# Optimization experiments

Hardware: AMD Instinct MI355X
Metric: run time of the kernel (lower is better)

The kernel has to match this reference:

```python
import jax, jax.numpy as jnp
import numpy as np

B, T, I, H, O, P = 32, 8192, 16, 128, 3, 1024


def setup_inputs() -> dict:
    key = jax.random.key(0)
    ks = jax.random.split(key, 8)
    x = jax.random.normal(ks[0], (B, T, I), dtype=jnp.float32)
    # feature channel 2 holds the photo id (original code does x[:,:,2].long())
    ids = jax.random.randint(ks[1], (B, T), 0, P)
    x = x.at[:, :, 2].set(ids.astype(jnp.float32))
    s = 1.0 / np.sqrt(H).astype(np.float32)
    W_ih = jax.random.uniform(ks[2], (4 * H, I), minval=-s, maxval=s, dtype=jnp.float32)
    W_hh = jax.random.uniform(ks[3], (4 * H, H), minval=-s, maxval=s, dtype=jnp.float32)
    b_ih = jax.random.uniform(ks[4], (4 * H,), minval=-s, maxval=s, dtype=jnp.float32)
    b_hh = jax.random.uniform(ks[5], (4 * H,), minval=-s, maxval=s, dtype=jnp.float32)
    W_fc = jax.random.uniform(ks[6], (O, H), minval=-s, maxval=s, dtype=jnp.float32)
    b_fc = jax.random.uniform(ks[7], (O,), minval=-s, maxval=s, dtype=jnp.float32)
    return dict(x=x, W_ih=W_ih, W_hh=W_hh, b_ih=b_ih, b_hh=b_hh,
                W_fc=W_fc, b_fc=b_fc, num_photos=P)


def _lstm(x, W_ih, W_hh, b_ih, b_hh):
    # single-layer batch_first LSTM, PyTorch gate order (i, f, g, o), zero init state
    Bz = x.shape[0]
    Hh = W_hh.shape[1]
    # precompute input contribution for all timesteps: [B, T, 4H]
    xg = jnp.einsum('bti,gi->btg', x, W_ih) + b_ih + b_hh

    def step(carry, gx):
        h, c = carry
        g = gx + h @ W_hh.T
        i, f, gg, o = jnp.split(g, 4, axis=-1)
        i = jax.nn.sigmoid(i)
        f = jax.nn.sigmoid(f)
        gg = jnp.tanh(gg)
        o = jax.nn.sigmoid(o)
        c = f * c + i * gg
        h = o * jnp.tanh(c)
        return (h, c), h

    h0 = jnp.zeros((Bz, Hh), x.dtype)
    _, hs = jax.lax.scan(step, (h0, h0), jnp.swapaxes(xg, 0, 1))  # [T, B, H]
    return jnp.swapaxes(hs, 0, 1)  # [B, T, H]


def reference(x, W_ih, W_hh, b_ih, b_hh, W_fc, b_fc, num_photos):
    Bz, T, _ = x.shape
    h = _lstm(x, W_ih, W_hh, b_ih, b_hh)          # [B, T, H]
    out = h @ W_fc.T + b_fc                        # [B, T, 3]
    ids = x[:, :, 2].astype(jnp.int32)             # [B, T]
    valid = ids < num_photos
    safe = jnp.where(valid, ids, 0)
    # flatten (batch, photo_id) into a single segment id per element
    seg = (jnp.arange(Bz, dtype=jnp.int32)[:, None] * num_photos + safe).reshape(-1)
    w = valid.astype(out.dtype)
    sums = jax.ops.segment_sum((out * w[..., None]).reshape(-1, out.shape[-1]),
                               seg, num_segments=Bz * num_photos)
    sums = sums.reshape(Bz, num_photos, out.shape[-1])
    counts = jax.ops.segment_sum(w.reshape(-1), seg, num_segments=Bz * num_photos)
    counts = counts.reshape(Bz, num_photos, 1)
    counts = jnp.where(counts == 0, 1.0, counts)   # matches photo_counts[photo_counts==0]=1
    return sums / counts
```

## Files before the change

### kernel.cpp

```cpp
#include <hip/hip_runtime.h>

#define B_ 32
#define T_ 8192
#define I_ 16
#define H_ 128
#define P_ 1024
#define O_ 3

typedef _Float16 h2 __attribute__((ext_vector_type(2)));
typedef _Float16 h4 __attribute__((ext_vector_type(4)));
typedef _Float16 h8 __attribute__((ext_vector_type(8)));

#if __has_builtin(__builtin_amdgcn_fdot2)
#define FDOT2(a, b, c) __builtin_amdgcn_fdot2((a), (b), (c), false)
#else
__device__ __forceinline__ float fdot2_asm(h2 a, h2 b, float c) {
    asm("v_dot2_f32_f16 %0, %1, %2, %0" : "+v"(c) : "v"(a), "v"(b));
    return c;
}
#define FDOT2(a, b, c) fdot2_asm((a), (b), (c))
#endif

#define FORME(M, g) M(g,0,0) M(g,0,1) M(g,0,2) M(g,0,3) \
                    M(g,1,0) M(g,1,1) M(g,1,2) M(g,1,3) \
                    M(g,2,0) M(g,2,1) M(g,2,2) M(g,2,3) \
                    M(g,3,0) M(g,3,1) M(g,3,2) M(g,3,3)
#define FORALL(M) FORME(M,0) FORME(M,1) FORME(M,2) FORME(M,3)
#define FORG(M) M(0) M(1) M(2) M(3)

#define DPPF(v, ctrl) \
    __int_as_float(__builtin_amdgcn_mov_dpp(__float_as_int(v), (ctrl), 0xF, 0xF, true))
#define SWZF(v, imm) \
    __int_as_float(__builtin_amdgcn_ds_swizzle(__float_as_int(v), (imm)))

__device__ __forceinline__ float tanh_f(float x) {
    return 2.f / (1.f + __expf(-2.f * x)) - 1.f;
}
__device__ __forceinline__ h4 cvt4(float4 v) {
    return (h4){(_Float16)v.x, (_Float16)v.y, (_Float16)v.z, (_Float16)v.w};
}

__device__ __forceinline__ void lds_barrier() {
    asm volatile("s_waitcnt lgkmcnt(0)\n\ts_barrier" ::: "memory");
}

__global__ __launch_bounds__(512, 2) __attribute__((amdgpu_waves_per_eu(2, 2)))
void lstm_fused(
    const float* __restrict__ x,
    const float* __restrict__ W_ih,
    const float* __restrict__ W_hh,
    const float* __restrict__ b_ih,
    const float* __restrict__ b_hh,
    const float* __restrict__ W_fc,
    float* __restrict__ sums,
    float* __restrict__ counts)
{
    const int b   = blockIdx.x;
    const int tid = threadIdx.x;
    const int j   = tid >> 2;
    const int kc  = tid & 3;

    __shared__ __align__(16) _Float16 hh[2][H_];
    __shared__ __align__(16) _Float16 xt[2][16 * I_];
    __shared__ float sums_lds[P_ * O_];
    __shared__ float counts_lds[P_];

    const float* wr0 = W_hh + (0 * H_ + j) * H_;
    const float* wr1 = W_hh + (1 * H_ + j) * H_;
    const float* wr2 = W_hh + (2 * H_ + j) * H_;
    const float* wr3 = W_hh + (3 * H_ + j) * H_;
    #define WLOAD(g, m, e) h2 W##g##_##m##_##e = (h2){ \
        (_Float16)wr##g[kc * 8 + 32 * (m) + 2 * (e)], \
        (_Float16)wr##g[kc * 8 + 32 * (m) + 2 * (e) + 1]};
    FORALL(WLOAD)

    #define ULOAD(g) \
        h2 U##g##_0 = (h2){(_Float16)W_ih[((g) * H_ + j) * I_ + kc * 4 + 0], \
                           (_Float16)W_ih[((g) * H_ + j) * I_ + kc * 4 + 1]}; \
        h2 U##g##_1 = (h2){(_Float16)W_ih[((g) * H_ + j) * I_ + kc * 4 + 2], \
                           (_Float16)W_ih[((g) * H_ + j) * I_ + kc * 4 + 3]};
    FORG(ULOAD)

    const float bias = b_ih[kc * H_ + j] + b_hh[kc * H_ + j];
    const float wfc  = (kc < 3) ? W_fc[kc * H_ + j] : 0.f;

    for (int i = tid; i < P_ * O_; i += 512) sums_lds[i] = 0.f;
    for (int i = tid; i < P_;      i += 512) counts_lds[i] = 0.f;
    if (tid < H_) hh[0][tid] = (_Float16)0.f;

    const float* xb = x + (size_t)b * T_ * I_;
    float4 xr4 = make_float4(0.f, 0.f, 0.f, 0.f);
    if (tid < 64) {
        xr4 = ((const float4*)xb)[tid];
        *(h4*)&xt[0][tid * 4] = cvt4(xr4);
    }
    float c = 0.f;
    __syncthreads();

    #pragma unroll 1
    for (int t = 0; t < T_; ++t) {
        const int off = t & 15;
        const int btx = (t >> 4) & 1;
        const int bh  = t & 1;

        if (tid < 64) {
            if (off == 0 && t + 16 < T_)
                xr4 = ((const float4*)(xb + (t + 16) * I_))[tid];
            if (off == 8 && t + 8 < T_)
                *(h4*)&xt[btx ^ 1][tid * 4] = cvt4(xr4);
        }

        const h4 xv4 = *(const h4*)&xt[btx][off * I_ + kc * 4];
        const h2 xv0 = __builtin_shufflevector(xv4, xv4, 0, 1);
        const h2 xv1 = __builtin_shufflevector(xv4, xv4, 2, 3);
        const int id = (int)(float)xt[btx][off * I_ + 2];

        float acc0 = 0.f, acc1 = 0.f, acc2 = 0.f, acc3 = 0.f;
        #define HD(m) { \
            h8 hv = *(const h8*)&hh[bh][kc * 8 + 32 * (m)]; \
            h2 p0 = __builtin_shufflevector(hv, hv, 0, 1); \
            h2 p1 = __builtin_shufflevector(hv, hv, 2, 3); \
            h2 p2 = __builtin_shufflevector(hv, hv, 4, 5); \
            h2 p3 = __builtin_shufflevector(hv, hv, 6, 7); \
            acc0 = FDOT2(p0, W0_##m##_0, acc0); acc0 = FDOT2(p1, W0_##m##_1, acc0); \
            acc0 = FDOT2(p2, W0_##m##_2, acc0); acc0 = FDOT2(p3, W0_##m##_3, acc0); \
            acc1 = FDOT2(p0, W1_##m##_0, acc1); acc1 = FDOT2(p1, W1_##m##_1, acc1); \
            acc1 = FDOT2(p2, W1_##m##_2, acc1); acc1 = FDOT2(p3, W1_##m##_3, acc1); \
            acc2 = FDOT2(p0, W2_##m##_0, acc2); acc2 = FDOT2(p1, W2_##m##_1, acc2); \
            acc2 = FDOT2(p2, W2_##m##_2, acc2); acc2 = FDOT2(p3, W2_##m##_3, acc2); \
            acc3 = FDOT2(p0, W3_##m##_0, acc3); acc3 = FDOT2(p1, W3_##m##_1, acc3); \
            acc3 = FDOT2(p2, W3_##m##_2, acc3); acc3 = FDOT2(p3, W3_##m##_3, acc3); }
        HD(0) HD(1) HD(2) HD(3)
        acc0 = FDOT2(xv0, U0_0, acc0); acc0 = FDOT2(xv1, U0_1, acc0);
        acc1 = FDOT2(xv0, U1_0, acc1); acc1 = FDOT2(xv1, U1_1, acc1);
        acc2 = FDOT2(xv0, U2_0, acc2); acc2 = FDOT2(xv1, U2_1, acc2);
        acc3 = FDOT2(xv0, U3_0, acc3); acc3 = FDOT2(xv1, U3_1, acc3);

        float s_;
        s_ = DPPF(acc0, 0xB1); acc0 += s_;
        s_ = DPPF(acc1, 0xB1); acc1 += s_;
        s_ = DPPF(acc2, 0xB1); acc2 += s_;
        s_ = DPPF(acc3, 0xB1); acc3 += s_;
        s_ = DPPF(acc0, 0x4E); acc0 += s_;
        s_ = DPPF(acc1, 0x4E); acc1 += s_;
        s_ = DPPF(acc2, 0x4E); acc2 += s_;
        s_ = DPPF(acc3, 0x4E); acc3 += s_;

        float tg = (kc == 0) ? acc0 : (kc == 1) ? acc1 : (kc == 2) ? acc2 : acc3;
        tg += bias;
        const bool  isg = (kc == 2);
        const float arg = isg ? (tg + tg) : tg;
        const float sf  = 1.f / (1.f + __expf(-arg));
        const float act = isg ? (sf + sf - 1.f) : sf;

        const float gi = DPPF(act, 0x00);
        const float gf = DPPF(act, 0x55);
        const float gg = DPPF(act, 0xAA);
        const float go = DPPF(act, 0xFF);
        c = fmaf(gf, c, gi * gg);
        const float hnew = go * tanh_f(c);

        if (kc == 0) hh[bh ^ 1][j] = (_Float16)hnew;

        float p = hnew * wfc;
        p += SWZF(p, 0x101F);
        p += SWZF(p, 0x201F);
        p += SWZF(p, 0x401F);
        p += __shfl_xor(p, 32, 64);
        const bool idv = ((unsigned)id < P_);
        if (((tid & 63) < 3) && idv)
            atomicAdd(&sums_lds[id * O_ + (tid & 63)], p);
        if (tid == 0 && idv)
            atomicAdd(&counts_lds[id], 1.f);

        lds_barrier();
    }

    float* sums_g = sums + (size_t)b * P_ * O_;
    for (int i = tid; i < P_ * O_; i += 512) sums_g[i] = sums_lds[i];
    float* cnt_g = counts + (size_t)b * P_;
    for (int i = tid; i < P_; i += 512) cnt_g[i] = counts_lds[i];
}

__global__ void finalize_kernel(const float* __restrict__ sums,
                                const float* __restrict__ counts,
                                const float* __restrict__ b_fc,
                                float* __restrict__ out)
{
    const int idx = blockIdx.x * blockDim.x + threadIdx.x;
    if (idx >= B_ * P_ * O_) return;
    const int o  = idx % O_;
    const int bp = idx / O_;
    const float cnt = counts[bp];
    const float denom = (cnt > 0.f) ? cnt : 1.f;
    out[idx] = (sums[idx] + cnt * b_fc[o]) / denom;
}

extern "C" void kernel_launch(void* const* d_in, const int* in_sizes, int n_in,
                              void* d_out, int out_size, void* d_ws, size_t ws_size,
                              hipStream_t stream) {
    const float* x    = (const float*)d_in[0];
    const float* W_ih = (const float*)d_in[1];
    const float* W_hh = (const float*)d_in[2];
    const float* b_ih = (const float*)d_in[3];
    const float* b_hh = (const float*)d_in[4];
    const float* W_fc = (const float*)d_in[5];
    const float* b_fc = (const float*)d_in[6];

    float* out    = (float*)d_out;
    float* sums   = (float*)d_ws;
    float* counts = sums + (size_t)B_ * P_ * O_;

    lstm_fused<<<B_, 512, 0, stream>>>(x, W_ih, W_hh, b_ih, b_hh, W_fc, sums, counts);

    const int n = B_ * P_ * O_;
    finalize_kernel<<<(n + 255) / 256, 256, 0, stream>>>(sums, counts, b_fc, out);
}
```

Baseline: 6.357 ms.

## Process two batch sequences per block with interleaved LSTM recurrences

Each block now runs two independent batch sequences, launched on 16 blocks instead of 32. Both recurrences are interleaved in one step loop so their dot products and reductions can hide each other's latency, and both share one barrier per timestep. The photo counts move out of the recurrent loop into a separate small count kernel. The trade-off is half as many blocks and roughly double the work per step, which may lengthen each serial step.

```diff
diff --git a/kernel.cpp b/kernel.cpp
--- a/kernel.cpp
+++ b/kernel.cpp
@@ -6,6 +6,7 @@
 #define H_ 128
 #define P_ 1024
 #define O_ 3
+#define NB 16
 
 typedef _Float16 h2 __attribute__((ext_vector_type(2)));
 typedef _Float16 h4 __attribute__((ext_vector_type(4)));
@@ -30,6 +31,7 @@
 
 #define DPPF(v, ctrl) \
     __int_as_float(__builtin_amdgcn_mov_dpp(__float_as_int(v), (ctrl), 0xF, 0xF, true))
+#define DPPI(v, ctrl) __builtin_amdgcn_mov_dpp((v), (ctrl), 0xF, 0xF, true)
 #define SWZF(v, imm) \
     __int_as_float(__builtin_amdgcn_ds_swizzle(__float_as_int(v), (imm)))
 
@@ -44,7 +46,7 @@
     asm volatile("s_waitcnt lgkmcnt(0)\n\ts_barrier" ::: "memory");
 }
 
-__global__ __launch_bounds__(512, 2) __attribute__((amdgpu_waves_per_eu(2, 2)))
+__global__ __launch_bounds__(512, 2)
 void lstm_fused(
     const float* __restrict__ x,
     const float* __restrict__ W_ih,
@@ -52,18 +54,22 @@
     const float* __restrict__ b_ih,
     const float* __restrict__ b_hh,
     const float* __restrict__ W_fc,
-    float* __restrict__ sums,
-    float* __restrict__ counts)
+    float* __restrict__ sums)
 {
-    const int b   = blockIdx.x;
-    const int tid = threadIdx.x;
-    const int j   = tid >> 2;
-    const int kc  = tid & 3;
-
-    __shared__ __align__(16) _Float16 hh[2][H_];
-    __shared__ __align__(16) _Float16 xt[2][16 * I_];
-    __shared__ float sums_lds[P_ * O_];
-    __shared__ float counts_lds[P_];
+    const int blk  = blockIdx.x;
+    const int tid  = threadIdx.x;
+    const int lane = tid & 63;
+    const int j    = tid >> 2;
+    const int kc   = tid & 3;
+    const int bA   = blk;
+    const int bB   = blk + NB;
+
+    __shared__ __align__(16) _Float16 hhA[2][H_];
+    __shared__ __align__(16) _Float16 hhB[2][H_];
+    __shared__ __align__(16) _Float16 xtA[2][16 * I_];
+    __shared__ __align__(16) _Float16 xtB[2][16 * I_];
+    __shared__ float sumsA_lds[P_ * O_];
+    __shared__ float sumsB_lds[P_ * O_];
 
     const float* wr0 = W_hh + (0 * H_ + j) * H_;
     const float* wr1 = W_hh + (1 * H_ + j) * H_;
@@ -73,7 +79,6 @@
         (_Float16)wr##g[kc * 8 + 32 * (m) + 2 * (e)], \
         (_Float16)wr##g[kc * 8 + 32 * (m) + 2 * (e) + 1]};
     FORALL(WLOAD)
-
     #define ULOAD(g) \
         h2 U##g##_0 = (h2){(_Float16)W_ih[((g) * H_ + j) * I_ + kc * 4 + 0], \
                            (_Float16)W_ih[((g) * H_ + j) * I_ + kc * 4 + 1]}; \
@@ -84,17 +89,16 @@
     const float bias = b_ih[kc * H_ + j] + b_hh[kc * H_ + j];
     const float wfc  = (kc < 3) ? W_fc[kc * H_ + j] : 0.f;
 
-    for (int i = tid; i < P_ * O_; i += 512) sums_lds[i] = 0.f;
-    for (int i = tid; i < P_;      i += 512) counts_lds[i] = 0.f;
-    if (tid < H_) hh[0][tid] = (_Float16)0.f;
-
-    const float* xb = x + (size_t)b * T_ * I_;
+    for (int i = tid; i < P_ * O_; i += 512) { sumsA_lds[i] = 0.f; sumsB_lds[i] = 0.f; }
+    if (tid < H_) { hhA[0][tid] = (_Float16)0.f; hhB[0][tid] = (_Float16)0.f; }
+
+    const float* xbA = x + (size_t)bA * T_ * I_;
+    const float* xbB = x + (size_t)bB * T_ * I_;
     float4 xr4 = make_float4(0.f, 0.f, 0.f, 0.f);
-    if (tid < 64) {
-        xr4 = ((const float4*)xb)[tid];
-        *(h4*)&xt[0][tid * 4] = cvt4(xr4);
-    }
-    float c = 0.f;
+    const int wv = tid >> 6;
+    if (wv == 0) { xr4 = ((const float4*)xbA)[lane]; *(h4*)&xtA[0][lane * 4] = cvt4(xr4); }
+    if (wv == 1) { xr4 = ((const float4*)xbB)[lane]; *(h4*)&xtB[0][lane * 4] = cvt4(xr4); }
+    float cA = 0.f, cB = 0.f;
     __syncthreads();
 
     #pragma unroll 1
@@ -103,83 +107,129 @@
         const int btx = (t >> 4) & 1;
         const int bh  = t & 1;
 
-        if (tid < 64) {
-            if (off == 0 && t + 16 < T_)
-                xr4 = ((const float4*)(xb + (t + 16) * I_))[tid];
-            if (off == 8 && t + 8 < T_)
-                *(h4*)&xt[btx ^ 1][tid * 4] = cvt4(xr4);
+        if (wv == 0) {
+            if (off == 0 && t + 16 < T_) xr4 = ((const float4*)(xbA + (t + 16) * I_))[lane];
+            if (off == 8 && t + 8 < T_)  *(h4*)&xtA[btx ^ 1][lane * 4] = cvt4(xr4);
+        } else if (wv == 1) {
+            if (off == 0 && t + 16 < T_) xr4 = ((const float4*)(xbB + (t + 16) * I_))[lane];
+            if (off == 8 && t + 8 < T_)  *(h4*)&xtB[btx ^ 1][lane * 4] = cvt4(xr4);
         }
 
-        const h4 xv4 = *(const h4*)&xt[btx][off * I_ + kc * 4];
-        const h2 xv0 = __builtin_shufflevector(xv4, xv4, 0, 1);
-        const h2 xv1 = __builtin_shufflevector(xv4, xv4, 2, 3);
-        const int id = (int)(float)xt[btx][off * I_ + 2];
-
-        float acc0 = 0.f, acc1 = 0.f, acc2 = 0.f, acc3 = 0.f;
-        #define HD(m) { \
-            h8 hv = *(const h8*)&hh[bh][kc * 8 + 32 * (m)]; \
-            h2 p0 = __builtin_shufflevector(hv, hv, 0, 1); \
-            h2 p1 = __builtin_shufflevector(hv, hv, 2, 3); \
-            h2 p2 = __builtin_shufflevector(hv, hv, 4, 5); \
-            h2 p3 = __builtin_shufflevector(hv, hv, 6, 7); \
-            acc0 = FDOT2(p0, W0_##m##_0, acc0); acc0 = FDOT2(p1, W0_##m##_1, acc0); \
-            acc0 = FDOT2(p2, W0_##m##_2, acc0); acc0 = FDOT2(p3, W0_##m##_3, acc0); \
-            acc1 = FDOT2(p0, W1_##m##_0, acc1); acc1 = FDOT2(p1, W1_##m##_1, acc1); \
-            acc1 = FDOT2(p2, W1_##m##_2, acc1); acc1 = FDOT2(p3, W1_##m##_3, acc1); \
-            acc2 = FDOT2(p0, W2_##m##_0, acc2); acc2 = FDOT2(p1, W2_##m##_1, acc2); \
-            acc2 = FDOT2(p2, W2_##m##_2, acc2); acc2 = FDOT2(p3, W2_##m##_3, acc2); \
-            acc3 = FDOT2(p0, W3_##m##_0, acc3); acc3 = FDOT2(p1, W3_##m##_1, acc3); \
-            acc3 = FDOT2(p2, W3_##m##_2, acc3); acc3 = FDOT2(p3, W3_##m##_3, acc3); }
-        HD(0) HD(1) HD(2) HD(3)
-        acc0 = FDOT2(xv0, U0_0, acc0); acc0 = FDOT2(xv1, U0_1, acc0);
-        acc1 = FDOT2(xv0, U1_0, acc1); acc1 = FDOT2(xv1, U1_1, acc1);
-        acc2 = FDOT2(xv0, U2_0, acc2); acc2 = FDOT2(xv1, U2_1, acc2);
-        acc3 = FDOT2(xv0, U3_0, acc3); acc3 = FDOT2(xv1, U3_1, acc3);
+        const h4 xA4 = *(const h4*)&xtA[btx][off * I_ + kc * 4];
+        const h4 xB4 = *(const h4*)&xtB[btx][off * I_ + kc * 4];
+        const h2 xA0 = __builtin_shufflevector(xA4, xA4, 0, 1);
+        const h2 xA1 = __builtin_shufflevector(xA4, xA4, 2, 3);
+        const h2 xB0 = __builtin_shufflevector(xB4, xB4, 0, 1);
+        const h2 xB1 = __builtin_shufflevector(xB4, xB4, 2, 3);
+        int idA = (int)(float)xA4[2]; idA = DPPI(idA, 0x00);
+        int idB = (int)(float)xB4[2]; idB = DPPI(idB, 0x00);
+
+        float a0A = 0.f, a1A = 0.f, a2A = 0.f, a3A = 0.f;
+        float a0B = 0.f, a1B = 0.f, a2B = 0.f, a3B = 0.f;
+        #define HD2(m) { \
+            h8 hA = *(const h8*)&hhA[bh][kc * 8 + 32 * (m)]; \
+            h8 hB = *(const h8*)&hhB[bh][kc * 8 + 32 * (m)]; \
+            h2 pA0 = __builtin_shufflevector(hA, hA, 0, 1); \
+            h2 pA1 = __builtin_shufflevector(hA, hA, 2, 3); \
+            h2 pA2 = __builtin_shufflevector(hA, hA, 4, 5); \
+            h2 pA3 = __builtin_shufflevector(hA, hA, 6, 7); \
+            h2 pB0 = __builtin_shufflevector(hB, hB, 0, 1); \
+            h2 pB1 = __builtin_shufflevector(hB, hB, 2, 3); \
+            h2 pB2 = __builtin_shufflevector(hB, hB, 4, 5); \
+            h2 pB3 = __builtin_shufflevector(hB, hB, 6, 7); \
+            a0A = FDOT2(pA0, W0_##m##_0, a0A); a0A = FDOT2(pA1, W0_##m##_1, a0A); \
+            a0A = FDOT2(pA2, W0_##m##_2, a0A); a0A = FDOT2(pA3, W0_##m##_3, a0A); \
+            a1A = FDOT2(pA0, W1_##m##_0, a1A); a1A = FDOT2(pA1, W1_##m##_1, a1A); \
+            a1A = FDOT2(pA2, W1_##m##_2, a1A); a1A = FDOT2(pA3, W1_##m##_3, a1A); \
+            a2A = FDOT2(pA0, W2_##m##_0, a2A); a2A = FDOT2(pA1, W2_##m##_1, a2A); \
+            a2A = FDOT2(pA2, W2_##m##_2, a2A); a2A = FDOT2(pA3, W2_##m##_3, a2A); \
+            a3A = FDOT2(pA0, W3_##m##_0, a3A); a3A = FDOT2(pA1, W3_##m##_1, a3A); \
+            a3A = FDOT2(pA2, W3_##m##_2, a3A); a3A = FDOT2(pA3, W3_##m##_3, a3A); \
+            a0B = FDOT2(pB0, W0_##m##_0, a0B); a0B = FDOT2(pB1, W0_##m##_1, a0B); \
+            a0B = FDOT2(pB2, W0_##m##_2, a0B); a0B = FDOT2(pB3, W0_##m##_3, a0B); \
+            a1B = FDOT2(pB0, W1_##m##_0, a1B); a1B = FDOT2(pB1, W1_##m##_1, a1B); \
+            a1B = FDOT2(pB2, W1_##m##_2, a1B); a1B = FDOT2(pB3, W1_##m##_3, a1B); \
+            a2B = FDOT2(pB0, W2_##m##_0, a2B); a2B = FDOT2(pB1, W2_##m##_1, a2B); \
+            a2B = FDOT2(pB2, W2_##m##_2, a2B); a2B = FDOT2(pB3, W2_##m##_3, a2B); \
+            a3B = FDOT2(pB0, W3_##m##_0, a3B); a3B = FDOT2(pB1, W3_##m##_1, a3B); \
+            a3B = FDOT2(pB2, W3_##m##_2, a3B); a3B = FDOT2(pB3, W3_##m##_3, a3B); }
+        HD2(0) HD2(1) HD2(2) HD2(3)
+        a0A = FDOT2(xA0, U0_0, a0A); a0A = FDOT2(xA1, U0_1, a0A);
+        a1A = FDOT2(xA0, U1_0, a1A); a1A = FDOT2(xA1, U1_1, a1A);
+        a2A = FDOT2(xA0, U2_0, a2A); a2A = FDOT2(xA1, U2_1, a2A);
+        a3A = FDOT2(xA0, U3_0, a3A); a3A = FDOT2(xA1, U3_1, a3A);
+        a0B = FDOT2(xB0, U0_0, a0B); a0B = FDOT2(xB1, U0_1, a0B);
+        a1B = FDOT2(xB0, U1_0, a1B); a1B = FDOT2(xB1, U1_1, a1B);
+        a2B = FDOT2(xB0, U2_0, a2B); a2B = FDOT2(xB1, U2_1, a2B);
+        a3B = FDOT2(xB0, U3_0, a3B); a3B = FDOT2(xB1, U3_1, a3B);
 
         float s_;
-        s_ = DPPF(acc0, 0xB1); acc0 += s_;
-        s_ = DPPF(acc1, 0xB1); acc1 += s_;
-        s_ = DPPF(acc2, 0xB1); acc2 += s_;
-        s_ = DPPF(acc3, 0xB1); acc3 += s_;
-        s_ = DPPF(acc0, 0x4E); acc0 += s_;
-        s_ = DPPF(acc1, 0x4E); acc1 += s_;
-        s_ = DPPF(acc2, 0x4E); acc2 += s_;
-        s_ = DPPF(acc3, 0x4E); acc3 += s_;
-
-        float tg = (kc == 0) ? acc0 : (kc == 1) ? acc1 : (kc == 2) ? acc2 : acc3;
-        tg += bias;
-        const bool  isg = (kc == 2);
-        const float arg = isg ? (tg + tg) : tg;
-        const float sf  = 1.f / (1.f + __expf(-arg));
-        const float act = isg ? (sf + sf - 1.f) : sf;
-
-        const float gi = DPPF(act, 0x00);
-        const float gf = DPPF(act, 0x55);
-        const float gg = DPPF(act, 0xAA);
-        const float go = DPPF(act, 0xFF);
-        c = fmaf(gf, c, gi * gg);
-        const float hnew = go * tanh_f(c);
-
-        if (kc == 0) hh[bh ^ 1][j] = (_Float16)hnew;
-
-        float p = hnew * wfc;
-        p += SWZF(p, 0x101F);
-        p += SWZF(p, 0x201F);
-        p += SWZF(p, 0x401F);
-        p += __shfl_xor(p, 32, 64);
-        const bool idv = ((unsigned)id < P_);
-        if (((tid & 63) < 3) && idv)
-            atomicAdd(&sums_lds[id * O_ + (tid & 63)], p);
-        if (tid == 0 && idv)
-            atomicAdd(&counts_lds[id], 1.f);
+        s_ = DPPF(a0A, 0xB1); a0A += s_;  s_ = DPPF(a0B, 0xB1); a0B += s_;
+        s_ = DPPF(a1A, 0xB1); a1A += s_;  s_ = DPPF(a1B, 0xB1); a1B += s_;
+        s_ = DPPF(a2A, 0xB1); a2A += s_;  s_ = DPPF(a2B, 0xB1); a2B += s_;
+        s_ = DPPF(a3A, 0xB1); a3A += s_;  s_ = DPPF(a3B, 0xB1); a3B += s_;
+        s_ = DPPF(a0A, 0x4E); a0A += s_;  s_ = DPPF(a0B, 0x4E); a0B += s_;
+        s_ = DPPF(a1A, 0x4E); a1A += s_;  s_ = DPPF(a1B, 0x4E); a1B += s_;
+        s_ = DPPF(a2A, 0x4E); a2A += s_;  s_ = DPPF(a2B, 0x4E); a2B += s_;
+        s_ = DPPF(a3A, 0x4E); a3A += s_;  s_ = DPPF(a3B, 0x4E); a3B += s_;
+
+        const bool isg = (kc == 2);
+        float tgA = (kc == 0) ? a0A : (kc == 1) ? a1A : (kc == 2) ? a2A : a3A;
+        float tgB = (kc == 0) ? a0B : (kc == 1) ? a1B : (kc == 2) ? a2B : a3B;
+        tgA += bias; tgB += bias;
+        const float argA = isg ? (tgA + tgA) : tgA;
+        const float argB = isg ? (tgB + tgB) : tgB;
+        const float sfA = 1.f / (1.f + __expf(-argA));
+        const float sfB = 1.f / (1.f + __expf(-argB));
+        const float actA = isg ? (sfA + sfA - 1.f) : sfA;
+        const float actB = isg ? (sfB + sfB - 1.f) : sfB;
+
+        const float giA = DPPF(actA, 0x00), giB = DPPF(actB, 0x00);
+        const float gfA = DPPF(actA, 0x55), gfB = DPPF(actB, 0x55);
+        const float ggA = DPPF(actA, 0xAA), ggB = DPPF(actB, 0xAA);
+        const float goA = DPPF(actA, 0xFF), goB = DPPF(actB, 0xFF);
+        cA = fmaf(gfA, cA, giA * ggA);
+        cB = fmaf(gfB, cB, giB * ggB);
+        const float hnA = goA * tanh_f(cA);
+        const float hnB = goB * tanh_f(cB);
+
+        if (kc == 0) { hhA[bh ^ 1][j] = (_Float16)hnA; hhB[bh ^ 1][j] = (_Float16)hnB; }
+
+        float pA = hnA * wfc;
+        float pB = hnB * wfc;
+        pA += SWZF(pA, 0x101F);  pB += SWZF(pB, 0x101F);
+        pA += SWZF(pA, 0x201F);  pB += SWZF(pB, 0x201F);
+        pA += SWZF(pA, 0x401F);  pB += SWZF(pB, 0x401F);
+        pA += __shfl_xor(pA, 32, 64);
+        pB += __shfl_xor(pB, 32, 64);
+        const bool red = (lane < 3);
+        if (red && (unsigned)idA < P_) atomicAdd(&sumsA_lds[idA * O_ + lane], pA);
+        if (red && (unsigned)idB < P_) atomicAdd(&sumsB_lds[idB * O_ + lane], pB);
 
         lds_barrier();
     }
 
-    float* sums_g = sums + (size_t)b * P_ * O_;
-    for (int i = tid; i < P_ * O_; i += 512) sums_g[i] = sums_lds[i];
-    float* cnt_g = counts + (size_t)b * P_;
-    for (int i = tid; i < P_; i += 512) cnt_g[i] = counts_lds[i];
+    __syncthreads();
+    float* sgA = sums + (size_t)bA * P_ * O_;
+    float* sgB = sums + (size_t)bB * P_ * O_;
+    for (int i = tid; i < P_ * O_; i += 512) { sgA[i] = sumsA_lds[i]; sgB[i] = sumsB_lds[i]; }
+}
+
+__global__ void count_kernel(const float* __restrict__ x,
+                             float* __restrict__ counts)
+{
+    const int b = blockIdx.x;
+    __shared__ int cnt[P_];
+    for (int i = threadIdx.x; i < P_; i += 256) cnt[i] = 0;
+    __syncthreads();
+    const float* xb = x + (size_t)b * T_ * I_;
+    for (int t = threadIdx.x; t < T_; t += 256) {
+        const int id = (int)xb[t * I_ + 2];
+        if ((unsigned)id < P_) atomicAdd(&cnt[id], 1);
+    }
+    __syncthreads();
+    for (int i = threadIdx.x; i < P_; i += 256)
+        counts[b * P_ + i] = (float)cnt[i];
 }
 
 __global__ void finalize_kernel(const float* __restrict__ sums,
@@ -211,7 +261,8 @@
     float* sums   = (float*)d_ws;
     float* counts = sums + (size_t)B_ * P_ * O_;
 
-    lstm_fused<<<B_, 512, 0, stream>>>(x, W_ih, W_hh, b_ih, b_hh, W_fc, sums, counts);
+    lstm_fused<<<NB, 512, 0, stream>>>(x, W_ih, W_hh, b_ih, b_hh, W_fc, sums);
+    count_kernel<<<B_, 256, 0, stream>>>(x, counts);
 
     const int n = B_ * P_ * O_;
     finalize_kernel<<<(n + 255) / 256, 256, 0, stream>>>(sums, counts, b_fc, out);
```

After: 11.08 ms. +74.2%, slower.
